# Optimization experiments

Hardware: AMD Instinct MI355X
Metric: run time of the kernel (lower is better)

The kernel has to match this reference:

```python
import jax, jax.numpy as jnp
import numpy as np

B, T, V, E, U = 256, 512, 20000, 128, 128


def setup_inputs() -> dict:
    key = jax.random.key(0)
    k = jax.random.split(key, 7)
    tokens = jax.random.randint(k[0], (B, T), 0, V)
    emb_table = jax.random.normal(k[1], (V, E), jnp.float32) * 0.05
    kernel = jax.random.normal(k[2], (E, 4 * U), jnp.float32) * 0.05
    recurrent_kernel = jax.random.normal(k[3], (U, 4 * U), jnp.float32) * 0.05
    # Keras default: unit_forget_bias -> forget-gate bias = 1, others 0 (gate order i,f,c,o)
    bias = jnp.concatenate([jnp.zeros(U), jnp.ones(U), jnp.zeros(2 * U)]).astype(jnp.float32)
    dense_w = jax.random.normal(k[4], (U, 1), jnp.float32) * 0.05
    dense_b = jnp.zeros((1,), jnp.float32)
    return {"tokens": tokens, "emb_table": emb_table, "kernel": kernel,
            "recurrent_kernel": recurrent_kernel, "bias": bias,
            "dense_w": dense_w, "dense_b": dense_b}


def reference(tokens, emb_table, kernel, recurrent_kernel, bias, dense_w, dense_b):
    # Embedding lookup: [B,T] -> [B,T,E]
    x = emb_table[tokens]
    # Precompute input projections for all timesteps: [B,T,4U]
    zx = jnp.einsum('bte,eg->btg', x, kernel) + bias

    def step(carry, z_t):
        h, c = carry
        z = z_t + h @ recurrent_kernel          # [B,4U]
        i, f, g, o = jnp.split(z, 4, axis=-1)   # Keras gate order i,f,c,o
        i = jax.nn.sigmoid(i)
        f = jax.nn.sigmoid(f)
        g = jnp.tanh(g)
        o = jax.nn.sigmoid(o)
        c = f * c + i * g
        h = o * jnp.tanh(c)
        return (h, c), None

    h0 = jnp.zeros((tokens.shape[0], U), zx.dtype)
    c0 = jnp.zeros((tokens.shape[0], U), zx.dtype)
    (h_final, _), _ = jax.lax.scan(step, (h0, c0), jnp.swapaxes(zx, 0, 1))
    # Dense sigmoid head: [B,1]
    return jax.nn.sigmoid(h_final @ dense_w + dense_b)
```

## Files before the change

### kernel.cpp

```cpp
#include <hip/hip_runtime.h>
#include <hip/hip_bf16.h>

#define BB 256
#define TT 512
#define VV 20000
#define EE 128
#define UU 128
#define G4 512

typedef _Float16 f16x8 __attribute__((ext_vector_type(8)));
typedef float    f32x4 __attribute__((ext_vector_type(4)));

__device__ __forceinline__ float sigmoid_f(float x) {
    float e = __expf(-x);
    return __builtin_amdgcn_rcpf(1.0f + e);
}
__device__ __forceinline__ float tanh_f(float x) {
    float e = __expf(2.0f * x);
    return 1.0f - 2.0f * __builtin_amdgcn_rcpf(e + 1.0f);
}

__global__ __launch_bounds__(512, 2) void proj_kernel(
    const float* __restrict__ emb, const float* __restrict__ wk,
    const float* __restrict__ bias, float* __restrict__ P) {
    const int col = threadIdx.x;
    const int v0  = blockIdx.x * 16;

    __shared__ float elds[16 * EE];
    ((float4*)elds)[col] = ((const float4*)(emb + (size_t)v0 * EE))[col];
    __syncthreads();

    float bcol = bias[col];
    float acc[16];
#pragma unroll
    for (int r = 0; r < 16; ++r) acc[r] = bcol;

    const float4* elds4 = (const float4*)elds;
    for (int e0 = 0; e0 < EE; e0 += 4) {
        float k0 = wk[(e0 + 0) * G4 + col];
        float k1 = wk[(e0 + 1) * G4 + col];
        float k2 = wk[(e0 + 2) * G4 + col];
        float k3 = wk[(e0 + 3) * G4 + col];
#pragma unroll
        for (int r = 0; r < 16; ++r) {
            float4 ev = elds4[r * 32 + (e0 >> 2)];
            acc[r] = fmaf(ev.x, k0, acc[r]);
            acc[r] = fmaf(ev.y, k1, acc[r]);
            acc[r] = fmaf(ev.z, k2, acc[r]);
            acc[r] = fmaf(ev.w, k3, acc[r]);
        }
    }
#pragma unroll
    for (int r = 0; r < 16; ++r)
        P[(size_t)(v0 + r) * G4 + col] = acc[r];
}

__global__ __launch_bounds__(512, 2) void lstm_kernel(
    const int* __restrict__ tokens, const float* __restrict__ rk,
    const float* __restrict__ P, const float* __restrict__ dense_w,
    const float* __restrict__ dense_b, float* __restrict__ out) {
    const int tid = threadIdx.x;
    const int w   = tid >> 6;
    const int l   = tid & 63;
    const int j   = l & 15;
    const int kq  = l >> 4;
    const int b   = blockIdx.x;
    const int ucol = 16 * w + j;

    __shared__ __align__(16) _Float16 hbuf[2][UU];
    __shared__ float red[8];

    f16x8 bf[4][4];
#pragma unroll
    for (int kt = 0; kt < 4; ++kt) {
#pragma unroll
        for (int g = 0; g < 4; ++g) {
            f16x8 v;
#pragma unroll
            for (int i = 0; i < 8; ++i) {
                v[i] = (_Float16)rk[(size_t)(32 * kt + 8 * kq + i) * G4
                                    + g * 128 + ucol];
            }
            bf[kt][g] = v;
        }
    }

    if (tid < UU) hbuf[0][tid] = (_Float16)0.f;
    float c_state = 0.f, hv = 0.f;

    const int* trow = tokens + (size_t)b * TT;
    float pv[4];
    {
        int tok0 = trow[0];
#pragma unroll
        for (int g = 0; g < 4; ++g)
            pv[g] = P[(size_t)tok0 * G4 + g * 128 + ucol];
    }
    __syncthreads();

    for (int t = 0; t < TT; ++t) {
        int tokn = trow[(t + 1 < TT) ? (t + 1) : (TT - 1)];
        float pvn[4];
#pragma unroll
        for (int g = 0; g < 4; ++g)
            pvn[g] = P[(size_t)tokn * G4 + g * 128 + ucol];

        f16x8 af[4];
#pragma unroll
        for (int kt = 0; kt < 4; ++kt)
            af[kt] = *(const f16x8*)&hbuf[t & 1][32 * kt + 8 * kq];

        f32x4 acc[4];
#pragma unroll
        for (int g = 0; g < 4; ++g) acc[g] = (f32x4){pv[g], pv[g], pv[g], pv[g]};
#pragma unroll
        for (int kt = 0; kt < 4; ++kt) {
#pragma unroll
            for (int g = 0; g < 4; ++g)
                acc[g] = __builtin_amdgcn_mfma_f32_16x16x32_f16(
                             af[kt], bf[kt][g], acc[g], 0, 0, 0);
        }

        float gi = sigmoid_f(acc[0][0]);
        float gf = sigmoid_f(acc[1][0]);
        float gg = tanh_f(acc[2][0]);
        float go = sigmoid_f(acc[3][0]);
        c_state = fmaf(gf, c_state, gi * gg);
        hv      = go * tanh_f(c_state);

        if (kq == 0) hbuf[(t + 1) & 1][ucol] = (_Float16)hv;
#pragma unroll
        for (int g = 0; g < 4; ++g) pv[g] = pvn[g];
        __syncthreads();
    }

    float val = (kq == 0) ? hv * dense_w[ucol] : 0.f;
#pragma unroll
    for (int off = 32; off > 0; off >>= 1) val += __shfl_xor(val, off, 64);
    if (l == 0) red[w] = val;
    __syncthreads();
    if (tid == 0) {
        float s = dense_b[0];
#pragma unroll
        for (int i = 0; i < 8; ++i) s += red[i];
        out[b] = sigmoid_f(s);
    }
}

extern "C" void kernel_launch(void* const* d_in, const int* in_sizes, int n_in,
                              void* d_out, int out_size, void* d_ws, size_t ws_size,
                              hipStream_t stream) {
    const int*   tokens = (const int*)  d_in[0];
    const float* emb    = (const float*)d_in[1];
    const float* wk     = (const float*)d_in[2];
    const float* rk     = (const float*)d_in[3];
    const float* bias   = (const float*)d_in[4];
    const float* dw     = (const float*)d_in[5];
    const float* db     = (const float*)d_in[6];
    float* out = (float*)d_out;
    float* P   = (float*)d_ws;

    proj_kernel<<<VV / 16, 512, 0, stream>>>(emb, wk, bias, P);
    lstm_kernel<<<BB, 512, 0, stream>>>(tokens, rk, P, dw, db, out);
}
```

Baseline: 303.1 us.

## Split gate nonlinearities across lane quarters and prefetch projections two steps ahead

Each lane quarter (kq) now computes only one gate's activation, using a single sigmoid with tanh expressed as 2*sigmoid(2x)-1. The f, g and o values are gathered with cross-lane shuffles, replacing four redundant transcendentals per lane. Each lane loads one projected-input value per step instead of four, prefetched two steps ahead, and it is added after the MFMA chain rather than seeding the accumulators. The __syncthreads is replaced by an explicit lgkmcnt wait plus s_barrier. This shortens the serial per-step critical path, at the cost of added shuffle latency.

```diff
diff --git a/kernel.cpp b/kernel.cpp
--- a/kernel.cpp
+++ b/kernel.cpp
@@ -89,21 +89,16 @@
     float c_state = 0.f, hv = 0.f;
 
     const int* trow = tokens + (size_t)b * TT;
-    float pv[4];
-    {
-        int tok0 = trow[0];
-#pragma unroll
-        for (int g = 0; g < 4; ++g)
-            pv[g] = P[(size_t)tok0 * G4 + g * 128 + ucol];
-    }
+    const float* Pcol = P + (size_t)kq * 128 + ucol;
+    float pc = Pcol[(size_t)trow[0] * G4];
+    float pn = Pcol[(size_t)trow[1] * G4];
     __syncthreads();
 
+    const f32x4 cz = {0.f, 0.f, 0.f, 0.f};
+
     for (int t = 0; t < TT; ++t) {
-        int tokn = trow[(t + 1 < TT) ? (t + 1) : (TT - 1)];
-        float pvn[4];
-#pragma unroll
-        for (int g = 0; g < 4; ++g)
-            pvn[g] = P[(size_t)tokn * G4 + g * 128 + ucol];
+        int tok2 = trow[(t + 2 < TT) ? (t + 2) : (TT - 1)];
+        float p2 = Pcol[(size_t)tok2 * G4];
 
         f16x8 af[4];
 #pragma unroll
@@ -112,26 +107,35 @@
 
         f32x4 acc[4];
 #pragma unroll
-        for (int g = 0; g < 4; ++g) acc[g] = (f32x4){pv[g], pv[g], pv[g], pv[g]};
+        for (int g = 0; g < 4; ++g)
+            acc[g] = __builtin_amdgcn_mfma_f32_16x16x32_f16(af[0], bf[0][g], cz, 0, 0, 0);
 #pragma unroll
-        for (int kt = 0; kt < 4; ++kt) {
+        for (int kt = 1; kt < 4; ++kt) {
 #pragma unroll
             for (int g = 0; g < 4; ++g)
-                acc[g] = __builtin_amdgcn_mfma_f32_16x16x32_f16(
-                             af[kt], bf[kt][g], acc[g], 0, 0, 0);
+                acc[g] = __builtin_amdgcn_mfma_f32_16x16x32_f16(af[kt], bf[kt][g], acc[g], 0, 0, 0);
         }
 
-        float gi = sigmoid_f(acc[0][0]);
-        float gf = sigmoid_f(acc[1][0]);
-        float gg = tanh_f(acc[2][0]);
-        float go = sigmoid_f(acc[3][0]);
-        c_state = fmaf(gf, c_state, gi * gg);
-        hv      = go * tanh_f(c_state);
+        float z0 = acc[0][0], z1 = acc[1][0], z2 = acc[2][0], z3 = acc[3][0];
+        float zl = (kq & 2) ? ((kq & 1) ? z3 : z2) : ((kq & 1) ? z1 : z0);
+        zl += pc;
+
+        float xs = (kq == 2) ? zl + zl : zl;
+        float s  = sigmoid_f(xs);
+        float a  = (kq == 2) ? fmaf(2.f, s, -1.f) : s;
+
+        float fa = __shfl(a, j + 16, 64);
+        float ga = __shfl(a, j + 32, 64);
+        float oa = __shfl(a, j + 48, 64);
+
+        c_state = fmaf(fa, c_state, a * ga);
+        hv      = oa * tanh_f(c_state);
 
         if (kq == 0) hbuf[(t + 1) & 1][ucol] = (_Float16)hv;
-#pragma unroll
-        for (int g = 0; g < 4; ++g) pv[g] = pvn[g];
-        __syncthreads();
+        pc = pn; pn = p2;
+
+        asm volatile("s_waitcnt lgkmcnt(0)" ::: "memory");
+        __builtin_amdgcn_s_barrier();
     }
 
     float val = (kq == 0) ? hv * dense_w[ucol] : 0.f;
@@ -140,10 +144,10 @@
     if (l == 0) red[w] = val;
     __syncthreads();
     if (tid == 0) {
-        float s = dense_b[0];
+        float sum = dense_b[0];
 #pragma unroll
-        for (int i = 0; i < 8; ++i) s += red[i];
-        out[b] = sigmoid_f(s);
+        for (int i = 0; i < 8; ++i) sum += red[i];
+        out[b] = sigmoid_f(sum);
     }
 }
 
```

New measurement: 310.5 us. 1.02x slower.
